# Kernel tuning notes

Hardware: AMD Instinct MI355X
Metric: run time of the kernel (lower is better)

## Reference

```python
import jax, jax.numpy as jnp
import numpy as np

A = 2048        # atoms
D = 64          # depth (in_depth == out_depth)
FL = 12         # filter_length


def setup_inputs() -> dict:
    key = jax.random.key(0)
    k = jax.random.split(key, 7)
    return {
        "x": jax.random.normal(k[0], (A, D), dtype=jnp.float32),
        "connectivity": jax.random.uniform(k[1], (A, A, FL), dtype=jnp.float32),
        "bond_property": jax.random.normal(k[2], (A, FL, 2), dtype=jnp.float32),
        "pf0": jax.random.normal(k[3], (D, FL, D), dtype=jnp.float32) * 0.01,
        "bf0": jax.random.normal(k[4], (D, FL, 3), dtype=jnp.float32) * 0.01,
        "pf1": jax.random.normal(k[5], (D, FL, D), dtype=jnp.float32) * 0.01,
        "bf1": jax.random.normal(k[6], (D, FL, 3), dtype=jnp.float32) * 0.01,
    }


def _chem_conv(h, connectivity, bond_property, pf, bf):
    # h: (A, D); connectivity: (A, A_src, FL); pf: (O, FL, D); bf: (O, FL, 3)
    # node_connection[a,f,d] = sum_k connectivity[a,k,f] * h[k,d]
    node_conn = jnp.einsum('akf,kd->afd', connectivity, h)
    # bond_score[a,o,f] = sum_d node_conn[a,f,d] * pf[o,f,d]
    score = jnp.einsum('afd,ofd->aof', node_conn, pf)
    # combined = cat([score, bond_property], -1); out = sum over (f, 3) of combined * bf
    out = (jnp.einsum('aof,of->ao', score, bf[:, :, 0])
           + jnp.einsum('afc,ofc->ao', bond_property, bf[:, :, 1:3]))
    return out  # (A, O)


def reference(x, connectivity, bond_property, pf0, bf0, pf1, bf1):
    act = jax.nn.relu
    out = x
    for pf, bf in ((pf0, bf0), (pf1, bf1)):
        out = act(_chem_conv(out, connectivity, bond_property, pf, bf))
        out = _chem_conv(out, connectivity, bond_property, pf, bf) + x
        out = act(out)
    return out
```

## Files before the change

kernel.cpp:

```cpp
#include <hip/hip_runtime.h>
#include <hip/hip_bf16.h>

#define A_N   2048
#define D_N   64
#define FL_N  12
#define KTOT  (A_N * FL_N)
#define S_SPLIT 16
#define KCHUNK 1536
#define BKN   128
#define NBK   12
#define TILE_B 16384

typedef __attribute__((ext_vector_type(8))) short bf16x8;
typedef __attribute__((ext_vector_type(4))) short bf16x4;
typedef __attribute__((ext_vector_type(4))) float f32x4;

__device__ __forceinline__ short f2bf(float f) {
  union { __hip_bfloat16 b; short s; } u;
  u.b = __float2bfloat16(f);
  return u.s;
}

__global__ void k_setup_cvt(const float* __restrict__ pf0, const float* __restrict__ bf0,
                            const float* __restrict__ pf1, const float* __restrict__ bf1,
                            const float* __restrict__ bp, const float* __restrict__ x,
                            const float* __restrict__ conn,
                            short* __restrict__ P2_0, short* __restrict__ P2_1,
                            float* __restrict__ bond0, float* __restrict__ bond1,
                            short* __restrict__ xb, short* __restrict__ connb2) {
  int b = blockIdx.x, t = threadIdx.x;
  if (b >= 768) {
    size_t slot = (size_t)(b - 768) * 256 + t;
#pragma unroll
    for (int cc = 0; cc < 6; ++cc) {
      size_t i = (slot + (size_t)cc * 1048576) * 8;
      f32x4 a0 = __builtin_nontemporal_load((const f32x4*)(conn + i));
      f32x4 a1 = __builtin_nontemporal_load((const f32x4*)(conn + i + 4));
      bf16x8 v;
      v[0]=f2bf(a0[0]); v[1]=f2bf(a0[1]); v[2]=f2bf(a0[2]); v[3]=f2bf(a0[3]);
      v[4]=f2bf(a1[0]); v[5]=f2bf(a1[1]); v[6]=f2bf(a1[2]); v[7]=f2bf(a1[3]);
      int a = (int)(i / KTOT), c = (int)(i % KTOT);
      int rt = a >> 6, r = a & 63;
      int kc = c / KCHUNK, rem = c % KCHUNK;
      int bk = rem >> 7, k = rem & 127;
      size_t dst = ((size_t)((rt * 16 + kc) * NBK + bk) << 14) + (r << 8) + (k << 1);
      *(bf16x8*)((char*)connb2 + dst) = v;
    }
    return;
  }
  if (b < 192) {
    int idx = b * 256 + t;
    int f = (idx >> 6) % FL_N;
    int o = idx / (D_N * FL_N);
    P2_0[idx] = f2bf(pf0[idx] * bf0[(o * FL_N + f) * 3]);
    P2_1[idx] = f2bf(pf1[idx] * bf1[(o * FL_N + f) * 3]);
  } else if (b < 704) {
    int o = t & 63;
    int a = (b - 192) * 4 + (t >> 6);
    float s0 = 0.f, s1 = 0.f;
#pragma unroll
    for (int f = 0; f < FL_N; ++f) {
      float c0 = bp[(a * FL_N + f) * 2 + 0];
      float c1 = bp[(a * FL_N + f) * 2 + 1];
      s0 += c0 * bf0[(o * FL_N + f) * 3 + 1] + c1 * bf0[(o * FL_N + f) * 3 + 2];
      s1 += c0 * bf1[(o * FL_N + f) * 3 + 1] + c1 * bf1[(o * FL_N + f) * 3 + 2];
    }
    bond0[a * D_N + o] = s0;
    bond1[a * D_N + o] = s1;
  } else {
    int i = ((b - 704) * 256 + t) * 8;
    f32x4 a0 = *(const f32x4*)(x + i);
    f32x4 a1 = *(const f32x4*)(x + i + 4);
    bf16x8 v;
    v[0]=f2bf(a0[0]); v[1]=f2bf(a0[1]); v[2]=f2bf(a0[2]); v[3]=f2bf(a0[3]);
    v[4]=f2bf(a1[0]); v[5]=f2bf(a1[1]); v[6]=f2bf(a1[2]); v[7]=f2bf(a1[3]);
    *(bf16x8*)(xb + i) = v;
  }
}

__device__ __forceinline__ void prep_body(bf16x8 h0, bf16x8 h1,
                                          const short* __restrict__ P2,
                                          short* __restrict__ Bt2,
                                          int k0, int lane, int w) {
  int l15 = lane & 15, grp = lane >> 4;
  const short* prow = P2 + (w * 16 + l15) * (FL_N * D_N) + grp * 8;
  f32x4 acc[FL_N];
#pragma unroll
  for (int f = 0; f < FL_N; ++f) {
    bf16x8 p0 = *(const bf16x8*)(prow + f * D_N);
    bf16x8 p1 = *(const bf16x8*)(prow + f * D_N + 32);
    f32x4 c = {0.f, 0.f, 0.f, 0.f};
    c = __builtin_amdgcn_mfma_f32_16x16x32_bf16(p0, h0, c, 0, 0, 0);
    c = __builtin_amdgcn_mfma_f32_16x16x32_bf16(p1, h1, c, 0, 0, 0);
    acc[f] = c;
  }
#pragma unroll
  for (int r = 0; r < 4; ++r) {
    int o = w * 16 + grp * 4 + r;
    int katom = k0 + l15;
#pragma unroll
    for (int f = 0; f < FL_N; ++f) {
      int c = katom * FL_N + f;
      int kc = c / KCHUNK, rem = c % KCHUNK;
      int bk = rem >> 7, k = rem & 127;
      *(short*)((char*)Bt2 + ((size_t)(kc * NBK + bk) << 14) + (o << 8) + (k << 1))
          = f2bf(acc[f][r]);
    }
  }
}

__global__ void k_prep0(const short* __restrict__ xb, const short* __restrict__ P2,
                        short* __restrict__ Bt2) {
  int lane = threadIdx.x & 63, w = threadIdx.x >> 6;
  int l15 = lane & 15, grp = lane >> 4;
  int k0 = blockIdx.x * 16;
  const short* hrow = xb + (k0 + l15) * D_N + grp * 8;
  bf16x8 h0 = *(const bf16x8*)(hrow);
  bf16x8 h1 = *(const bf16x8*)(hrow + 32);
  prep_body(h0, h1, P2, Bt2, k0, lane, w);
}

template <int ADDX>
__global__ void k_prep_r(const float* __restrict__ part, const float* __restrict__ bond,
                         const float* __restrict__ x, const short* __restrict__ P2,
                         short* __restrict__ Bt2) {
  __shared__ short hsh[16 * 64];
  int t = threadIdx.x;
  int k0 = blockIdx.x * 16;
  int r  = t >> 4;
  int d0 = (t & 15) * 4;
  size_t base = (size_t)(k0 + r) * D_N + d0;
  f32x4 s = *(const f32x4*)(bond + base);
#pragma unroll
  for (int si = 0; si < S_SPLIT; ++si) {
    f32x4 p = *(const f32x4*)(part + (size_t)si * (A_N * D_N) + base);
    s[0] += p[0]; s[1] += p[1]; s[2] += p[2]; s[3] += p[3];
  }
  if (ADDX) {
    f32x4 xv = *(const f32x4*)(x + base);
    s[0] += xv[0]; s[1] += xv[1]; s[2] += xv[2]; s[3] += xv[3];
  }
  bf16x4 hv;
  hv[0] = f2bf(fmaxf(s[0], 0.f)); hv[1] = f2bf(fmaxf(s[1], 0.f));
  hv[2] = f2bf(fmaxf(s[2], 0.f)); hv[3] = f2bf(fmaxf(s[3], 0.f));
  *(bf16x4*)(&hsh[r * 64 + d0]) = hv;
  __syncthreads();
  int lane = t & 63, w = t >> 6, l15 = lane & 15, grp = lane >> 4;
  bf16x8 h0 = *(const bf16x8*)(&hsh[l15 * 64 + grp * 8]);
  bf16x8 h1 = *(const bf16x8*)(&hsh[l15 * 64 + grp * 8 + 32]);
  prep_body(h0, h1, P2, Bt2, k0, lane, w);
}

template <int C>
__global__ __launch_bounds__(256, 2) void k_gemm(const short* __restrict__ connb2,
                                                 const short* __restrict__ Bt2,
                                                 float* __restrict__ part) {
  __shared__ short lA[2][8192];
  __shared__ short lB[2][8192];
  int t = threadIdx.x;
  int lane = t & 63, w = t >> 6, l15 = lane & 15, grp = lane >> 4;
  int rt = blockIdx.x, kc = blockIdx.y;

  const char* Ab = (const char*)connb2 + (((size_t)(rt * 16 + kc) * NBK) << 14);
  const char* Bb = (const char*)Bt2 + (((size_t)kc * NBK) << 14);

  int ldsoff[4];
#pragma unroll
  for (int q = 0; q < 4; ++q) {
    int j = q * 256 + t;
    int row = j >> 4, cw = j & 15;
    ldsoff[q] = (row << 8) + ((cw << 4) ^ ((row & 7) << 4));
  }

  bf16x8 ra[4], rb[4];
#pragma unroll
  for (int q = 0; q < 4; ++q) {
    ra[q] = *(const bf16x8*)(Ab + q * 4096 + t * 16);
    rb[q] = *(const bf16x8*)(Bb + q * 4096 + t * 16);
  }
#pragma unroll
  for (int q = 0; q < 4; ++q) {
    *(bf16x8*)((char*)&lA[0][0] + ldsoff[q]) = ra[q];
    *(bf16x8*)((char*)&lB[0][0] + ldsoff[q]) = rb[q];
  }
  __syncthreads();

  f32x4 acc0 = {0,0,0,0}, acc1 = {0,0,0,0}, acc2 = {0,0,0,0}, acc3 = {0,0,0,0};
  const int arow = (w * 16 + l15) << 8;
  const int brow = l15 << 8;
  const int key  = (l15 & 7) << 4;

#pragma unroll
  for (int bk = 0; bk < NBK; ++bk) {
    const int cur = bk & 1;
    if (bk + 1 < NBK) {
      const char* An = Ab + (size_t)(bk + 1) * TILE_B;
      const char* Bn = Bb + (size_t)(bk + 1) * TILE_B;
#pragma unroll
      for (int q = 0; q < 4; ++q) {
        ra[q] = *(const bf16x8*)(An + q * 4096 + t * 16);
        rb[q] = *(const bf16x8*)(Bn + q * 4096 + t * 16);
      }
    }
    const char* la = (const char*)&lA[cur][0];
    const char* lb = (const char*)&lB[cur][0];
#pragma unroll
    for (int ks = 0; ks < 4; ++ks) {
      const int cb = ((ks << 6) + (grp << 4)) ^ key;
      bf16x8 af = *(const bf16x8*)(la + arow + cb);
      bf16x8 b0 = *(const bf16x8*)(lb + brow + cb);
      bf16x8 b1 = *(const bf16x8*)(lb + 4096 + brow + cb);
      bf16x8 b2 = *(const bf16x8*)(lb + 8192 + brow + cb);
      bf16x8 b3 = *(const bf16x8*)(lb + 12288 + brow + cb);
      acc0 = __builtin_amdgcn_mfma_f32_16x16x32_bf16(af, b0, acc0, 0, 0, 0);
      acc1 = __builtin_amdgcn_mfma_f32_16x16x32_bf16(af, b1, acc1, 0, 0, 0);
      acc2 = __builtin_amdgcn_mfma_f32_16x16x32_bf16(af, b2, acc2, 0, 0, 0);
      acc3 = __builtin_amdgcn_mfma_f32_16x16x32_bf16(af, b3, acc3, 0, 0, 0);
    }
    if (bk + 1 < NBK) {
      const int nxt = cur ^ 1;
#pragma unroll
      for (int q = 0; q < 4; ++q) {
        *(bf16x8*)((char*)&lA[nxt][0] + ldsoff[q]) = ra[q];
        *(bf16x8*)((char*)&lB[nxt][0] + ldsoff[q]) = rb[q];
      }
    }
    __syncthreads();
  }

  float* p = part + (size_t)kc * (A_N * D_N);
  int rbase = rt * 64 + w * 16 + grp * 4;
#pragma unroll
  for (int r = 0; r < 4; ++r) {
    float* pr = p + (size_t)(rbase + r) * D_N + l15;
    pr[0]  = acc0[r];
    pr[16] = acc1[r];
    pr[32] = acc2[r];
    pr[48] = acc3[r];
  }
}

__global__ void k_final(const float* __restrict__ part, const float* __restrict__ bond,
                        const float* __restrict__ x, float* __restrict__ out) {
  int i = blockIdx.x * 256 + threadIdx.x;
  float s = bond[i];
#pragma unroll
  for (int si = 0; si < S_SPLIT; ++si) s += part[(size_t)si * (A_N * D_N) + i];
  out[i] = fmaxf(s + x[i], 0.f);
}

extern "C" void kernel_launch(void* const* d_in, const int* in_sizes, int n_in,
                              void* d_out, int out_size, void* d_ws, size_t ws_size,
                              hipStream_t stream) {
  const float* x    = (const float*)d_in[0];
  const float* conn = (const float*)d_in[1];
  const float* bprp = (const float*)d_in[2];
  const float* pf0  = (const float*)d_in[3];
  const float* bf0  = (const float*)d_in[4];
  const float* pf1  = (const float*)d_in[5];
  const float* bf1  = (const float*)d_in[6];
  float* out = (float*)d_out;

  char* ws = (char*)d_ws;
  size_t off = 0;
  short* connb2 = (short*)(ws + off); off += (size_t)A_N * KTOT * 2;
  short* Bt2    = (short*)(ws + off); off += (size_t)D_N * KTOT * 2;
  float* part   = (float*)(ws + off); off += (size_t)S_SPLIT * A_N * D_N * 4;
  short* xb     = (short*)(ws + off); off += (size_t)A_N * D_N * 2;
  float* bond0  = (float*)(ws + off); off += (size_t)A_N * D_N * 4;
  float* bond1  = (float*)(ws + off); off += (size_t)A_N * D_N * 4;
  short* P2_0   = (short*)(ws + off); off += (size_t)D_N * FL_N * D_N * 2;
  short* P2_1   = (short*)(ws + off); off += (size_t)D_N * FL_N * D_N * 2;

  k_setup_cvt<<<4864, 256, 0, stream>>>(pf0, bf0, pf1, bf1, bprp, x, conn,
                                        P2_0, P2_1, bond0, bond1, xb, connb2);

  dim3 ggrid(32, 16);

  k_prep0<<<128, 256, 0, stream>>>(xb, P2_0, Bt2);
  k_gemm<0><<<ggrid, 256, 0, stream>>>(connb2, Bt2, part);

  k_prep_r<0><<<128, 256, 0, stream>>>(part, bond0, x, P2_0, Bt2);
  k_gemm<1><<<ggrid, 256, 0, stream>>>(connb2, Bt2, part);

  k_prep_r<1><<<128, 256, 0, stream>>>(part, bond0, x, P2_1, Bt2);
  k_gemm<2><<<ggrid, 256, 0, stream>>>(connb2, Bt2, part);

  k_prep_r<0><<<128, 256, 0, stream>>>(part, bond1, x, P2_1, Bt2);
  k_gemm<3><<<ggrid, 256, 0, stream>>>(connb2, Bt2, part);

  k_final<<<512, 256, 0, stream>>>(part, bond1, x, out);
}
```

Measured before the change: 182.7 us.

## Pre-swizzle GEMM operands into MFMA fragment order and drop LDS staging

The bf16 connectivity and B operand are now written in an order that matches the MFMA fragment layout, so each lane loads its A and B fragments straight from global memory into registers. The GEMM no longer stages tiles through double-buffered LDS, which removes the LDS writes, reads and barriers. The split-K factor doubles to 32 with shorter K chunks, and each wave computes 32 rows by 64 columns. The cost is twice as many fp32 partial sums for the prep and final kernels to write and reduce, and no on-chip reuse of the B fragments across the block's waves.

```diff
diff --git a/kernel.cpp b/kernel.cpp
--- a/kernel.cpp
+++ b/kernel.cpp
@@ -5,11 +5,11 @@
 #define D_N   64
 #define FL_N  12
 #define KTOT  (A_N * FL_N)
-#define S_SPLIT 16
-#define KCHUNK 1536
+#define S_SPLIT 32
+#define KCHUNK 768
 #define BKN   128
-#define NBK   12
-#define TILE_B 16384
+#define NBK   6
+
 
 typedef __attribute__((ext_vector_type(8))) short bf16x8;
 typedef __attribute__((ext_vector_type(4))) short bf16x4;
@@ -40,10 +40,13 @@
       v[0]=f2bf(a0[0]); v[1]=f2bf(a0[1]); v[2]=f2bf(a0[2]); v[3]=f2bf(a0[3]);
       v[4]=f2bf(a1[0]); v[5]=f2bf(a1[1]); v[6]=f2bf(a1[2]); v[7]=f2bf(a1[3]);
       int a = (int)(i / KTOT), c = (int)(i % KTOT);
-      int rt = a >> 6, r = a & 63;
-      int kc = c / KCHUNK, rem = c % KCHUNK;
-      int bk = rem >> 7, k = rem & 127;
-      size_t dst = ((size_t)((rt * 16 + kc) * NBK + bk) << 14) + (r << 8) + (k << 1);
+      int rt64 = a >> 6, r64 = a & 63;
+      int w_ = r64 >> 4, l15_ = r64 & 15;
+      int kc = c / KCHUNK; int krem = c - kc * KCHUNK;
+      int bk = krem >> 7, kk = krem & 127;
+      int ks = kk >> 5, g2 = (kk >> 3) & 3;
+      size_t dst = (((size_t)((rt64 * S_SPLIT + kc) * NBK + bk)) << 14)
+                   + ((w_ * 4 + ks) << 10) + ((g2 * 16 + l15_) << 4);
       *(bf16x8*)((char*)connb2 + dst) = v;
     }
     return;
@@ -98,12 +101,16 @@
   for (int r = 0; r < 4; ++r) {
     int o = w * 16 + grp * 4 + r;
     int katom = k0 + l15;
+    int j = o >> 4, lo = o & 15;
 #pragma unroll
     for (int f = 0; f < FL_N; ++f) {
       int c = katom * FL_N + f;
-      int kc = c / KCHUNK, rem = c % KCHUNK;
-      int bk = rem >> 7, k = rem & 127;
-      *(short*)((char*)Bt2 + ((size_t)(kc * NBK + bk) << 14) + (o << 8) + (k << 1))
+      int kc = c / KCHUNK;
+      int krem = c - kc * KCHUNK;
+      int bk = krem >> 7, kk = krem & 127;
+      int ks = kk >> 5, g2 = (kk >> 3) & 3, kin = kk & 7;
+      *(short*)((char*)Bt2 + (((size_t)(kc * NBK + bk)) << 14)
+                + ((j * 4 + ks) << 10) + ((g2 * 16 + lo) << 4) + (kin << 1))
           = f2bf(acc[f][r]);
     }
   }
@@ -155,88 +162,57 @@
 __global__ __launch_bounds__(256, 2) void k_gemm(const short* __restrict__ connb2,
                                                  const short* __restrict__ Bt2,
                                                  float* __restrict__ part) {
-  __shared__ short lA[2][8192];
-  __shared__ short lB[2][8192];
-  int t = threadIdx.x;
-  int lane = t & 63, w = t >> 6, l15 = lane & 15, grp = lane >> 4;
-  int rt = blockIdx.x, kc = blockIdx.y;
-
-  const char* Ab = (const char*)connb2 + (((size_t)(rt * 16 + kc) * NBK) << 14);
-  const char* Bb = (const char*)Bt2 + (((size_t)kc * NBK) << 14);
-
-  int ldsoff[4];
-#pragma unroll
-  for (int q = 0; q < 4; ++q) {
-    int j = q * 256 + t;
-    int row = j >> 4, cw = j & 15;
-    ldsoff[q] = (row << 8) + ((cw << 4) ^ ((row & 7) << 4));
-  }
-
-  bf16x8 ra[4], rb[4];
-#pragma unroll
-  for (int q = 0; q < 4; ++q) {
-    ra[q] = *(const bf16x8*)(Ab + q * 4096 + t * 16);
-    rb[q] = *(const bf16x8*)(Bb + q * 4096 + t * 16);
-  }
-#pragma unroll
-  for (int q = 0; q < 4; ++q) {
-    *(bf16x8*)((char*)&lA[0][0] + ldsoff[q]) = ra[q];
-    *(bf16x8*)((char*)&lB[0][0] + ldsoff[q]) = rb[q];
-  }
-  __syncthreads();
-
-  f32x4 acc0 = {0,0,0,0}, acc1 = {0,0,0,0}, acc2 = {0,0,0,0}, acc3 = {0,0,0,0};
-  const int arow = (w * 16 + l15) << 8;
-  const int brow = l15 << 8;
-  const int key  = (l15 & 7) << 4;
-
-#pragma unroll
+  int t = threadIdx.x, lane = t & 63, w = t >> 6, l15 = lane & 15, grp = lane >> 4;
+  int bid = blockIdx.x;
+  int rt = bid & 15, kc = bid >> 4;
+  int rowtile = rt * 2 + (w >> 1);
+  const int fwb = (w & 1) * 2;
+
+  const char* Abase = (const char*)connb2
+      + (((size_t)((rowtile * S_SPLIT + kc) * NBK)) << 14) + (lane << 4);
+  const char* Bbase = (const char*)Bt2
+      + (((size_t)(kc * NBK)) << 14) + (lane << 4);
+
+  f32x4 acc[2][4] = {};
+
+#pragma unroll 2
   for (int bk = 0; bk < NBK; ++bk) {
-    const int cur = bk & 1;
-    if (bk + 1 < NBK) {
-      const char* An = Ab + (size_t)(bk + 1) * TILE_B;
-      const char* Bn = Bb + (size_t)(bk + 1) * TILE_B;
-#pragma unroll
-      for (int q = 0; q < 4; ++q) {
-        ra[q] = *(const bf16x8*)(An + q * 4096 + t * 16);
-        rb[q] = *(const bf16x8*)(Bn + q * 4096 + t * 16);
-      }
-    }
-    const char* la = (const char*)&lA[cur][0];
-    const char* lb = (const char*)&lB[cur][0];
-#pragma unroll
-    for (int ks = 0; ks < 4; ++ks) {
-      const int cb = ((ks << 6) + (grp << 4)) ^ key;
-      bf16x8 af = *(const bf16x8*)(la + arow + cb);
-      bf16x8 b0 = *(const bf16x8*)(lb + brow + cb);
-      bf16x8 b1 = *(const bf16x8*)(lb + 4096 + brow + cb);
-      bf16x8 b2 = *(const bf16x8*)(lb + 8192 + brow + cb);
-      bf16x8 b3 = *(const bf16x8*)(lb + 12288 + brow + cb);
-      acc0 = __builtin_amdgcn_mfma_f32_16x16x32_bf16(af, b0, acc0, 0, 0, 0);
-      acc1 = __builtin_amdgcn_mfma_f32_16x16x32_bf16(af, b1, acc1, 0, 0, 0);
-      acc2 = __builtin_amdgcn_mfma_f32_16x16x32_bf16(af, b2, acc2, 0, 0, 0);
-      acc3 = __builtin_amdgcn_mfma_f32_16x16x32_bf16(af, b3, acc3, 0, 0, 0);
-    }
-    if (bk + 1 < NBK) {
-      const int nxt = cur ^ 1;
-#pragma unroll
-      for (int q = 0; q < 4; ++q) {
-        *(bf16x8*)((char*)&lA[nxt][0] + ldsoff[q]) = ra[q];
-        *(bf16x8*)((char*)&lB[nxt][0] + ldsoff[q]) = rb[q];
-      }
-    }
-    __syncthreads();
+    const char* At = Abase + ((size_t)bk << 14);
+    const char* Bt = Bbase + ((size_t)bk << 14);
+    bf16x8 a[2][4], bfr[4][4];
+#pragma unroll
+    for (int rg = 0; rg < 2; ++rg)
+#pragma unroll
+      for (int ks = 0; ks < 4; ++ks)
+        a[rg][ks] = __builtin_nontemporal_load(
+            (const bf16x8*)(At + (((fwb + rg) * 4 + ks) << 10)));
+#pragma unroll
+    for (int j = 0; j < 4; ++j)
+#pragma unroll
+      for (int ks = 0; ks < 4; ++ks)
+        bfr[j][ks] = *(const bf16x8*)(Bt + ((j * 4 + ks) << 10));
+#pragma unroll
+    for (int rg = 0; rg < 2; ++rg)
+#pragma unroll
+      for (int j = 0; j < 4; ++j)
+#pragma unroll
+        for (int ks = 0; ks < 4; ++ks)
+          acc[rg][j] = __builtin_amdgcn_mfma_f32_16x16x32_bf16(
+              a[rg][ks], bfr[j][ks], acc[rg][j], 0, 0, 0);
   }
 
   float* p = part + (size_t)kc * (A_N * D_N);
-  int rbase = rt * 64 + w * 16 + grp * 4;
-#pragma unroll
-  for (int r = 0; r < 4; ++r) {
-    float* pr = p + (size_t)(rbase + r) * D_N + l15;
-    pr[0]  = acc0[r];
-    pr[16] = acc1[r];
-    pr[32] = acc2[r];
-    pr[48] = acc3[r];
+#pragma unroll
+  for (int rg = 0; rg < 2; ++rg) {
+    int rbase = rowtile * 64 + (w & 1) * 32 + rg * 16 + grp * 4;
+#pragma unroll
+    for (int r = 0; r < 4; ++r) {
+      float* pr = p + (size_t)(rbase + r) * D_N + l15;
+      pr[0]  = acc[rg][0][r];
+      pr[16] = acc[rg][1][r];
+      pr[32] = acc[rg][2][r];
+      pr[48] = acc[rg][3][r];
+    }
   }
 }
 
@@ -275,19 +251,17 @@
   k_setup_cvt<<<4864, 256, 0, stream>>>(pf0, bf0, pf1, bf1, bprp, x, conn,
                                         P2_0, P2_1, bond0, bond1, xb, connb2);
 
-  dim3 ggrid(32, 16);
-
   k_prep0<<<128, 256, 0, stream>>>(xb, P2_0, Bt2);
-  k_gemm<0><<<ggrid, 256, 0, stream>>>(connb2, Bt2, part);
+  k_gemm<0><<<512, 256, 0, stream>>>(connb2, Bt2, part);
 
   k_prep_r<0><<<128, 256, 0, stream>>>(part, bond0, x, P2_0, Bt2);
-  k_gemm<1><<<ggrid, 256, 0, stream>>>(connb2, Bt2, part);
+  k_gemm<1><<<512, 256, 0, stream>>>(connb2, Bt2, part);
 
   k_prep_r<1><<<128, 256, 0, stream>>>(part, bond0, x, P2_1, Bt2);
-  k_gemm<2><<<ggrid, 256, 0, stream>>>(connb2, Bt2, part);
+  k_gemm<2><<<512, 256, 0, stream>>>(connb2, Bt2, part);
 
   k_prep_r<0><<<128, 256, 0, stream>>>(part, bond1, x, P2_1, Bt2);
-  k_gemm<3><<<ggrid, 256, 0, stream>>>(connb2, Bt2, part);
+  k_gemm<3><<<512, 256, 0, stream>>>(connb2, Bt2, part);
 
   k_final<<<512, 256, 0, stream>>>(part, bond1, x, out);
 }
```

After: 293.4 us. +60.5%, slower.

## Pre-swizzle GEMM operands in global memory and load tiles directly into LDS

Applied to the files above, without the earlier changes.

The conversion and prep kernels now write connectivity and B operands with the XOR bank swizzle already applied in global memory. The GEMM then uses global_load_lds to copy tiles straight into shared memory, with no round trip through registers and no separate LDS stores. The aim is to cut VGPR pressure and the per-thread store instructions in the inner loop. The risk is correctness of the double buffering: the direct LDS loads are asynchronous, the only wait before they are read is the block barrier, and the barrier after the last iteration was removed.

```diff
diff --git a/kernel.cpp b/kernel.cpp
--- a/kernel.cpp
+++ b/kernel.cpp
@@ -7,7 +7,6 @@
 #define KTOT  (A_N * FL_N)
 #define S_SPLIT 16
 #define KCHUNK 1536
-#define BKN   128
 #define NBK   12
 #define TILE_B 16384
 
@@ -19,6 +18,12 @@
   union { __hip_bfloat16 b; short s; } u;
   u.b = __float2bfloat16(f);
   return u.s;
+}
+
+__device__ __forceinline__ void gload16(const void* g, void* l) {
+  __builtin_amdgcn_global_load_lds(
+      (const __attribute__((address_space(1))) unsigned int*)g,
+      (__attribute__((address_space(3))) unsigned int*)l, 16, 0, 0);
 }
 
 __global__ void k_setup_cvt(const float* __restrict__ pf0, const float* __restrict__ bf0,
@@ -43,7 +48,8 @@
       int rt = a >> 6, r = a & 63;
       int kc = c / KCHUNK, rem = c % KCHUNK;
       int bk = rem >> 7, k = rem & 127;
-      size_t dst = ((size_t)((rt * 16 + kc) * NBK + bk) << 14) + (r << 8) + (k << 1);
+      int cw = ((k >> 3) ^ (r & 7));
+      size_t dst = ((size_t)((rt * 16 + kc) * NBK + bk) << 14) + (r << 8) + (cw << 4);
       *(bf16x8*)((char*)connb2 + dst) = v;
     }
     return;
@@ -102,8 +108,10 @@
     for (int f = 0; f < FL_N; ++f) {
       int c = katom * FL_N + f;
       int kc = c / KCHUNK, rem = c % KCHUNK;
-      int bk = rem >> 7, k = rem & 127;
-      *(short*)((char*)Bt2 + ((size_t)(kc * NBK + bk) << 14) + (o << 8) + (k << 1))
+      int bk = rem >> 7, kk = rem & 127;
+      int cw = ((kk >> 3) ^ (o & 7));
+      *(short*)((char*)Bt2 + ((size_t)(kc * NBK + bk) << 14)
+                + (o << 8) + (cw << 4) + ((kk & 7) << 1))
           = f2bf(acc[f][r]);
     }
   }
@@ -163,25 +171,13 @@
 
   const char* Ab = (const char*)connb2 + (((size_t)(rt * 16 + kc) * NBK) << 14);
   const char* Bb = (const char*)Bt2 + (((size_t)kc * NBK) << 14);
-
-  int ldsoff[4];
+  const int wq = w << 10;
+  const int lane16 = lane << 4;
+
 #pragma unroll
   for (int q = 0; q < 4; ++q) {
-    int j = q * 256 + t;
-    int row = j >> 4, cw = j & 15;
-    ldsoff[q] = (row << 8) + ((cw << 4) ^ ((row & 7) << 4));
-  }
-
-  bf16x8 ra[4], rb[4];
-#pragma unroll
-  for (int q = 0; q < 4; ++q) {
-    ra[q] = *(const bf16x8*)(Ab + q * 4096 + t * 16);
-    rb[q] = *(const bf16x8*)(Bb + q * 4096 + t * 16);
-  }
-#pragma unroll
-  for (int q = 0; q < 4; ++q) {
-    *(bf16x8*)((char*)&lA[0][0] + ldsoff[q]) = ra[q];
-    *(bf16x8*)((char*)&lB[0][0] + ldsoff[q]) = rb[q];
+    gload16(Ab + q * 4096 + wq + lane16, (char*)&lA[0][0] + q * 4096 + wq);
+    gload16(Bb + q * 4096 + wq + lane16, (char*)&lB[0][0] + q * 4096 + wq);
   }
   __syncthreads();
 
@@ -193,13 +189,14 @@
 #pragma unroll
   for (int bk = 0; bk < NBK; ++bk) {
     const int cur = bk & 1;
+    const int nxt = cur ^ 1;
     if (bk + 1 < NBK) {
       const char* An = Ab + (size_t)(bk + 1) * TILE_B;
       const char* Bn = Bb + (size_t)(bk + 1) * TILE_B;
 #pragma unroll
       for (int q = 0; q < 4; ++q) {
-        ra[q] = *(const bf16x8*)(An + q * 4096 + t * 16);
-        rb[q] = *(const bf16x8*)(Bn + q * 4096 + t * 16);
+        gload16(An + q * 4096 + wq + lane16, (char*)&lA[nxt][0] + q * 4096 + wq);
+        gload16(Bn + q * 4096 + wq + lane16, (char*)&lB[nxt][0] + q * 4096 + wq);
       }
     }
     const char* la = (const char*)&lA[cur][0];
@@ -217,15 +214,7 @@
       acc2 = __builtin_amdgcn_mfma_f32_16x16x32_bf16(af, b2, acc2, 0, 0, 0);
       acc3 = __builtin_amdgcn_mfma_f32_16x16x32_bf16(af, b3, acc3, 0, 0, 0);
     }
-    if (bk + 1 < NBK) {
-      const int nxt = cur ^ 1;
-#pragma unroll
-      for (int q = 0; q < 4; ++q) {
-        *(bf16x8*)((char*)&lA[nxt][0] + ldsoff[q]) = ra[q];
-        *(bf16x8*)((char*)&lB[nxt][0] + ldsoff[q]) = rb[q];
-      }
-    }
-    __syncthreads();
+    if (bk + 1 < NBK) __syncthreads();
   }
 
   float* p = part + (size_t)kc * (A_N * D_N);
@@ -275,7 +264,7 @@
   k_setup_cvt<<<4864, 256, 0, stream>>>(pf0, bf0, pf1, bf1, bprp, x, conn,
                                         P2_0, P2_1, bond0, bond1, xb, connb2);
 
-  dim3 ggrid(32, 16);
+  dim3 ggrid(32, S_SPLIT);
 
   k_prep0<<<128, 256, 0, stream>>>(xb, P2_0, Bt2);
   k_gemm<0><<<ggrid, 256, 0, stream>>>(connb2, Bt2, part);
```

Result: no change. 185.8 us (+1.7%).
